# Optimization experiments

Hardware: AMD Instinct MI355X
Metric: run time of the kernel (lower is better)

## Reference

```python
import jax, jax.numpy as jnp
import numpy as np


def setup_inputs() -> dict:
    key = jax.random.key(0)
    ks = jax.random.split(key, 8)
    B, T, D, H, Z = 128, 512, 256, 1024, 128
    s_in = 1.0 / np.sqrt(D + H)
    s_h = 1.0 / np.sqrt(H)
    return {
        "x": jax.random.normal(ks[0], (B, T, D), jnp.float32),
        "W": jax.random.normal(ks[1], (D, 4 * H), jnp.float32) * s_in,
        "U": jax.random.normal(ks[2], (H, 4 * H), jnp.float32) * s_in,
        "b": jnp.zeros((4 * H,), jnp.float32),
        "Wm": jax.random.normal(ks[3], (H, Z), jnp.float32) * s_h,
        "bm": jnp.zeros((Z,), jnp.float32),
        "Wv": jax.random.normal(ks[4], (H, Z), jnp.float32) * s_h,
        "bv": jnp.zeros((Z,), jnp.float32),
        "eps": jax.random.normal(ks[5], (B, Z), jnp.float32),
    }


def reference(x, W, U, b, Wm, bm, Wv, bv, eps):
    # Keras LSTM with activation='softplus' (cell/output act), recurrent_activation=sigmoid.
    # Gate order in Keras kernels: i, f, c(g), o.
    B = x.shape[0]
    H = U.shape[0]

    def step(carry, xt):
        h, c = carry
        gates = xt @ W + h @ U + b  # [B, 4H]
        i, f, g, o = jnp.split(gates, 4, axis=-1)
        i = jax.nn.sigmoid(i)
        f = jax.nn.sigmoid(f)
        o = jax.nn.sigmoid(o)
        g = jax.nn.softplus(g)
        c_new = f * c + i * g
        h_new = o * jax.nn.softplus(c_new)
        return (h_new, c_new), None

    init = (jnp.zeros((B, H), x.dtype), jnp.zeros((B, H), x.dtype))
    (h_last, _), _ = jax.lax.scan(step, init, jnp.swapaxes(x, 0, 1))

    mu = h_last @ Wm + bm        # [B, Z]
    logvar = h_last @ Wv + bv    # [B, Z]
    z = mu + eps * jnp.exp(0.5 * logvar)  # reparameterization
    return mu, logvar, z
```

## Files before the change

kernel.cpp:

```cpp
#include <hip/hip_runtime.h>
#include <hip/hip_bf16.h>
#include <stdint.h>

#define NB 128
#define NT 512
#define ND 256
#define NH 1024
#define NZ 128
#define NG 4096

typedef __attribute__((ext_vector_type(8))) __bf16 bf16x8;
typedef __attribute__((ext_vector_type(4))) __bf16 bf16x4;
typedef __attribute__((ext_vector_type(4))) float floatx4;

__device__ __forceinline__ float fsigmoid_(float x) {
  return __fdividef(1.0f, 1.0f + __expf(-x));
}
__device__ __forceinline__ float fsoftplus_(float x) {
  return fmaxf(x, 0.0f) + __logf(1.0f + __expf(-fabsf(x)));
}

__device__ __forceinline__ bf16x8 load_bfrag(const float* s) {
  bf16x8 v;
#pragma unroll
  for (int jj = 0; jj < 8; ++jj) v[jj] = (__bf16)s[jj * NG];
  return v;
}

__global__ __launch_bounds__(256) void convert_x_kernel(
    const float4* __restrict__ x, __bf16* __restrict__ xb) {
  int i = blockIdx.x * 256 + threadIdx.x;
  int d4 = i & 63;
  int bt = i >> 6;
  int b = bt >> 9;
  int t = bt & 511;
  float4 v = x[i];
  bf16x4 o;
  o[0] = (__bf16)v.x; o[1] = (__bf16)v.y; o[2] = (__bf16)v.z; o[3] = (__bf16)v.w;
  *(bf16x4*)(xb + ((t * NB + b) * ND + d4 * 4)) = o;
}

__global__ __launch_bounds__(512, 1) void lstm_persistent(
    const __bf16* __restrict__ xb,
    const float* __restrict__ W,
    const float* __restrict__ U,
    const float* __restrict__ bias,
    __bf16* __restrict__ hbuf,
    float* __restrict__ hlast)
{
  const int tid = threadIdx.x;
  const int wg = blockIdx.x;
  const int m_blk = wg & 7;
  const int n_blk = wg >> 3;
  const int wave = tid >> 6;
  const int lane = tid & 63;
  const int q = lane >> 4;
  const int n16 = lane & 15;

  __shared__ float Gs[2][8][16][132];

#define AL(p) __hip_atomic_load(p, __ATOMIC_RELAXED, __HIP_MEMORY_SCOPE_AGENT)
#define AS(p, v) __hip_atomic_store(p, v, __ATOMIC_RELAXED, __HIP_MEMORY_SCOPE_AGENT)
#define MFMA_(a, b, acc) __builtin_amdgcn_mfma_f32_16x16x32_bf16(a, b, acc, 0, 0, 0)

  const int nb = n_blk * 32 + n16;
  const int c00 = nb,            c01 = nb + 16;
  const int c10 = NH + nb,       c11 = NH + nb + 16;
  const int c20 = 2 * NH + nb,   c21 = 2 * NH + nb + 16;
  const int c30 = 3 * NH + nb,   c31 = 3 * NH + nb + 16;

  const float* Wb = W + (wave * 32 + q * 8) * NG;
  bf16x8 BX00 = load_bfrag(Wb + c00), BX01 = load_bfrag(Wb + c01);
  bf16x8 BX10 = load_bfrag(Wb + c10), BX11 = load_bfrag(Wb + c11);
  bf16x8 BX20 = load_bfrag(Wb + c20), BX21 = load_bfrag(Wb + c21);
  bf16x8 BX30 = load_bfrag(Wb + c30), BX31 = load_bfrag(Wb + c31);
  const float* Ub = U + (wave * 128 + q * 8) * NG;
#define DECL_J(J)                                                       \
  bf16x8 BH00##J = load_bfrag(Ub + (J) * 32 * NG + c00);                \
  bf16x8 BH01##J = load_bfrag(Ub + (J) * 32 * NG + c01);                \
  bf16x8 BH10##J = load_bfrag(Ub + (J) * 32 * NG + c10);                \
  bf16x8 BH11##J = load_bfrag(Ub + (J) * 32 * NG + c11);                \
  bf16x8 BH20##J = load_bfrag(Ub + (J) * 32 * NG + c20);                \
  bf16x8 BH21##J = load_bfrag(Ub + (J) * 32 * NG + c21);                \
  bf16x8 BH30##J = load_bfrag(Ub + (J) * 32 * NG + c30);                \
  bf16x8 BH31##J = load_bfrag(Ub + (J) * 32 * NG + c31);
  DECL_J(0) DECL_J(1) DECL_J(2) DECL_J(3)
#undef DECL_J

  const float b00 = (wave == 0) ? bias[c00] : 0.f;
  const float b01 = (wave == 0) ? bias[c01] : 0.f;
  const float b10 = (wave == 0) ? bias[c10] : 0.f;
  const float b11 = (wave == 0) ? bias[c11] : 0.f;
  const float b20 = (wave == 0) ? bias[c20] : 0.f;
  const float b21 = (wave == 0) ? bias[c21] : 0.f;
  const float b30 = (wave == 0) ? bias[c30] : 0.f;
  const float b31 = (wave == 0) ? bias[c31] : 0.f;

  const int r_e = tid >> 5;
  const int c_e = tid & 31;
  const int hcol = n_blk * 32 + c_e;
  const int grow = m_blk * 16 + r_e;
  float c_state = 0.0f;

  const int goff = (m_blk * 16 + n16) * NH + (wave << 7) + (q << 3);

  floatx4 AC00, AC01, AC10, AC11, AC20, AC21, AC30, AC31;
#define XPHASE_(XA)                                                     \
  {                                                                     \
    AC00 = (floatx4){b00, b00, b00, b00}; AC01 = (floatx4){b01, b01, b01, b01}; \
    AC10 = (floatx4){b10, b10, b10, b10}; AC11 = (floatx4){b11, b11, b11, b11}; \
    AC20 = (floatx4){b20, b20, b20, b20}; AC21 = (floatx4){b21, b21, b21, b21}; \
    AC30 = (floatx4){b30, b30, b30, b30}; AC31 = (floatx4){b31, b31, b31, b31}; \
    AC00 = MFMA_(XA, BX00, AC00); AC01 = MFMA_(XA, BX01, AC01);         \
    AC10 = MFMA_(XA, BX10, AC10); AC11 = MFMA_(XA, BX11, AC11);         \
    AC20 = MFMA_(XA, BX20, AC20); AC21 = MFMA_(XA, BX21, AC21);         \
    AC30 = MFMA_(XA, BX30, AC30); AC31 = MFMA_(XA, BX31, AC31);         \
  }

#define XFRAG_PTR(T) (const bf16x8*)(xb + ((T) * NB + m_blk * 16 + n16) * ND \
                                     + wave * 32 + q * 8)

  {
    bf16x8 x0 = *XFRAG_PTR(0);
    XPHASE_(x0)
  }

  for (int t = 0; t < NT; ++t) {
    bf16x8 xv;
    if (t < NT - 1) xv = *XFRAG_PTR(t + 1);

    unsigned long long w0, w1, w2, w3, w4, w5, w6, w7;
    {
      const unsigned long long* hp =
          (const unsigned long long*)(hbuf + (t & 3) * (NB * NH) + goff);
      while (true) {
        w0 = AL(hp);      w1 = AL(hp + 1);
        w2 = AL(hp + 8);  w3 = AL(hp + 9);
        w4 = AL(hp + 16); w5 = AL(hp + 17);
        w6 = AL(hp + 24); w7 = AL(hp + 25);
        unsigned long long s =
            (w0 | w1 | w2 | w3 | w4 | w5 | w6 | w7) & 0x8000800080008000ULL;
        if (__all(s == 0ULL)) break;
        __builtin_amdgcn_s_sleep(1);
      }
    }
    union { unsigned long long u[2]; bf16x8 v; } u0, u1, u2, u3;
    u0.u[0] = w0; u0.u[1] = w1; u1.u[0] = w2; u1.u[1] = w3;
    u2.u[0] = w4; u2.u[1] = w5; u3.u[0] = w6; u3.u[1] = w7;
    bf16x8 a0 = u0.v, a1 = u1.v, a2 = u2.v, a3 = u3.v;

    AC00 = MFMA_(a0, BH000, AC00); AC01 = MFMA_(a0, BH010, AC01);
    AC10 = MFMA_(a0, BH100, AC10); AC11 = MFMA_(a0, BH110, AC11);
    AC20 = MFMA_(a0, BH200, AC20); AC21 = MFMA_(a0, BH210, AC21);
    AC30 = MFMA_(a0, BH300, AC30); AC31 = MFMA_(a0, BH310, AC31);
    AC00 = MFMA_(a1, BH001, AC00); AC01 = MFMA_(a1, BH011, AC01);
    AC10 = MFMA_(a1, BH101, AC10); AC11 = MFMA_(a1, BH111, AC11);
    AC20 = MFMA_(a1, BH201, AC20); AC21 = MFMA_(a1, BH211, AC21);
    AC30 = MFMA_(a1, BH301, AC30); AC31 = MFMA_(a1, BH311, AC31);
    AC00 = MFMA_(a2, BH002, AC00); AC01 = MFMA_(a2, BH012, AC01);
    AC10 = MFMA_(a2, BH102, AC10); AC11 = MFMA_(a2, BH112, AC11);
    AC20 = MFMA_(a2, BH202, AC20); AC21 = MFMA_(a2, BH212, AC21);
    AC30 = MFMA_(a2, BH302, AC30); AC31 = MFMA_(a2, BH312, AC31);
    AC00 = MFMA_(a3, BH003, AC00); AC01 = MFMA_(a3, BH013, AC01);
    AC10 = MFMA_(a3, BH103, AC10); AC11 = MFMA_(a3, BH113, AC11);
    AC20 = MFMA_(a3, BH203, AC20); AC21 = MFMA_(a3, BH213, AC21);
    AC30 = MFMA_(a3, BH303, AC30); AC31 = MFMA_(a3, BH313, AC31);

    const int gi = t & 1;
#pragma unroll
    for (int rr = 0; rr < 4; ++rr) {
      int row = q * 4 + rr;
      Gs[gi][wave][row][n16]       = AC00[rr];
      Gs[gi][wave][row][16 + n16]  = AC01[rr];
      Gs[gi][wave][row][32 + n16]  = AC10[rr];
      Gs[gi][wave][row][48 + n16]  = AC11[rr];
      Gs[gi][wave][row][64 + n16]  = AC20[rr];
      Gs[gi][wave][row][80 + n16]  = AC21[rr];
      Gs[gi][wave][row][96 + n16]  = AC30[rr];
      Gs[gi][wave][row][112 + n16] = AC31[rr];
    }

    __syncthreads();

    {
      float xi = 0.f, xf = 0.f, xg = 0.f, xo = 0.f;
#pragma unroll
      for (int w2i = 0; w2i < 8; ++w2i) {
        xi += Gs[gi][w2i][r_e][c_e];
        xf += Gs[gi][w2i][r_e][32 + c_e];
        xg += Gs[gi][w2i][r_e][64 + c_e];
        xo += Gs[gi][w2i][r_e][96 + c_e];
      }
      float iv = fsigmoid_(xi);
      float fv = fsigmoid_(xf);
      float gv = fsoftplus_(xg);
      float ov = fsigmoid_(xo);
      c_state = fv * c_state + iv * gv;
      float hv = ov * fsoftplus_(c_state);
      if (t == NT - 1) {
        hlast[grow * NH + hcol] = hv;
      } else {
        float hn1 = __shfl_xor(hv, 1);
        __hip_bfloat162 pk;
        pk.x = (__hip_bfloat16)hv; pk.y = (__hip_bfloat16)hn1;
        unsigned int pw = *(unsigned int*)&pk;
        unsigned int po = (unsigned int)__shfl_xor((int)pw, 2);
        if ((c_e & 3) == 0) {
          unsigned long long vv = ((unsigned long long)po << 32) | pw;
          AS((unsigned long long*)(hbuf + ((t + 1) & 3) * (NB * NH)
                                   + grow * NH + hcol), vv);
          AS((unsigned long long*)(hbuf + ((t + 3) & 3) * (NB * NH)
                                   + grow * NH + hcol),
             0xFFFFFFFFFFFFFFFFULL);
        }
      }
    }

    if (t < NT - 1) XPHASE_(xv)
  }
#undef XFRAG_PTR
#undef XPHASE_
#undef AS
#undef AL
#undef MFMA_
}

__global__ __launch_bounds__(128) void proj_kernel(
    const float* __restrict__ hlast,
    const float* __restrict__ Wm, const float* __restrict__ bm,
    const float* __restrict__ Wv, const float* __restrict__ bv,
    const float* __restrict__ eps, float* __restrict__ out) {
  __shared__ float hs[4][NH];
  const int bb = blockIdx.x * 4;
  for (int idx = threadIdx.x; idx < 4 * NH; idx += 128)
    hs[idx >> 10][idx & (NH - 1)] = hlast[(bb + (idx >> 10)) * NH + (idx & (NH - 1))];
  __syncthreads();
  const int z = threadIdx.x;
  float am[4] = {0.f, 0.f, 0.f, 0.f};
  float av[4] = {0.f, 0.f, 0.f, 0.f};
#pragma unroll 8
  for (int k = 0; k < NH; ++k) {
    float wm = Wm[k * NZ + z];
    float wv = Wv[k * NZ + z];
#pragma unroll
    for (int r = 0; r < 4; ++r) {
      am[r] += hs[r][k] * wm;
      av[r] += hs[r][k] * wv;
    }
  }
#pragma unroll
  for (int r = 0; r < 4; ++r) {
    int b = bb + r;
    float mu = am[r] + bm[z];
    float lv = av[r] + bv[z];
    float zz = mu + eps[b * NZ + z] * expf(0.5f * lv);
    out[b * NZ + z] = mu;
    out[NB * NZ + b * NZ + z] = lv;
    out[2 * NB * NZ + b * NZ + z] = zz;
  }
}

extern "C" void kernel_launch(void* const* d_in, const int* in_sizes, int n_in,
                              void* d_out, int out_size, void* d_ws, size_t ws_size,
                              hipStream_t stream) {
  const float* x   = (const float*)d_in[0];
  const float* W   = (const float*)d_in[1];
  const float* U   = (const float*)d_in[2];
  const float* b   = (const float*)d_in[3];
  const float* Wm  = (const float*)d_in[4];
  const float* bm  = (const float*)d_in[5];
  const float* Wv  = (const float*)d_in[6];
  const float* bv  = (const float*)d_in[7];
  const float* eps = (const float*)d_in[8];

  char* ws = (char*)d_ws;
  __bf16* hbuf = (__bf16*)ws;
  __bf16* xb   = (__bf16*)(ws + 1048576);
  float* hlast = (float*)(ws + 1048576);

  hipMemsetAsync(hbuf, 0, NB * NH * sizeof(__bf16), stream);
  hipMemsetAsync(hbuf + NB * NH, 0xFF, 3 * NB * NH * sizeof(__bf16), stream);

  convert_x_kernel<<<dim3((NB * NT * ND) / 4 / 256), dim3(256), 0, stream>>>(
      (const float4*)x, xb);

  void* args[] = {(void*)&xb, (void*)&W, (void*)&U, (void*)&b,
                  (void*)&hbuf, (void*)&hlast};
  hipLaunchCooperativeKernel(reinterpret_cast<void*>(lstm_persistent),
                             dim3(256), dim3(512), args, 0, stream);

  proj_kernel<<<dim3(32), dim3(128), 0, stream>>>(hlast, Wm, bm, Wv, bv, eps,
                                                  (float*)d_out);
}
```

Baseline: 2.415 ms.

## Split each workgroup's batch rows into two interleaved 8-row halves

Each workgroup now handles two 8-row batch groups (mA and mB) with separate accumulators and cell states, processing them one after the other within each timestep. While one half waits on its h dependency, the other half's producer group has time to finish, which is meant to hide cross-workgroup synchronization latency. Lanes with row index above 7 duplicate work in the MFMA (r8g = n16&7), so half the MFMA output is wasted. The polling loop also now reloads only the words still marked invalid. Costs include twice the accumulator registers and an extra __syncthreads per step.

```diff
diff --git a/kernel.cpp b/kernel.cpp
--- a/kernel.cpp
+++ b/kernel.cpp
@@ -50,14 +50,17 @@
 {
   const int tid = threadIdx.x;
   const int wg = blockIdx.x;
-  const int m_blk = wg & 7;
+  const int pp = wg & 7;
   const int n_blk = wg >> 3;
+  const int mA = pp;
+  const int mB = pp + 8;
   const int wave = tid >> 6;
   const int lane = tid & 63;
   const int q = lane >> 4;
   const int n16 = lane & 15;
-
-  __shared__ float Gs[2][8][16][132];
+  const int r8g = n16 & 7;
+
+  __shared__ float Gs[2][8][8][132];
 
 #define AL(p) __hip_atomic_load(p, __ATOMIC_RELAXED, __HIP_MEMORY_SCOPE_AGENT)
 #define AS(p, v) __hip_atomic_store(p, v, __ATOMIC_RELAXED, __HIP_MEMORY_SCOPE_AGENT)
@@ -96,130 +99,148 @@
   const float b30 = (wave == 0) ? bias[c30] : 0.f;
   const float b31 = (wave == 0) ? bias[c31] : 0.f;
 
-  const int r_e = tid >> 5;
-  const int c_e = tid & 31;
-  const int hcol = n_blk * 32 + c_e;
-  const int grow = m_blk * 16 + r_e;
-  float c_state = 0.0f;
-
-  const int goff = (m_blk * 16 + n16) * NH + (wave << 7) + (q << 3);
-
-  floatx4 AC00, AC01, AC10, AC11, AC20, AC21, AC30, AC31;
-#define XPHASE_(XA)                                                     \
+  float csA = 0.0f, csB = 0.0f;
+
+  floatx4 AA00, AA01, AA10, AA11, AA20, AA21, AA30, AA31;
+  floatx4 AB00, AB01, AB10, AB11, AB20, AB21, AB30, AB31;
+
+#define XPHASE_P(P, XA)                                                 \
   {                                                                     \
-    AC00 = (floatx4){b00, b00, b00, b00}; AC01 = (floatx4){b01, b01, b01, b01}; \
-    AC10 = (floatx4){b10, b10, b10, b10}; AC11 = (floatx4){b11, b11, b11, b11}; \
-    AC20 = (floatx4){b20, b20, b20, b20}; AC21 = (floatx4){b21, b21, b21, b21}; \
-    AC30 = (floatx4){b30, b30, b30, b30}; AC31 = (floatx4){b31, b31, b31, b31}; \
-    AC00 = MFMA_(XA, BX00, AC00); AC01 = MFMA_(XA, BX01, AC01);         \
-    AC10 = MFMA_(XA, BX10, AC10); AC11 = MFMA_(XA, BX11, AC11);         \
-    AC20 = MFMA_(XA, BX20, AC20); AC21 = MFMA_(XA, BX21, AC21);         \
-    AC30 = MFMA_(XA, BX30, AC30); AC31 = MFMA_(XA, BX31, AC31);         \
-  }
-
-#define XFRAG_PTR(T) (const bf16x8*)(xb + ((T) * NB + m_blk * 16 + n16) * ND \
-                                     + wave * 32 + q * 8)
+    P##00 = (floatx4){b00, b00, b00, b00}; P##01 = (floatx4){b01, b01, b01, b01}; \
+    P##10 = (floatx4){b10, b10, b10, b10}; P##11 = (floatx4){b11, b11, b11, b11}; \
+    P##20 = (floatx4){b20, b20, b20, b20}; P##21 = (floatx4){b21, b21, b21, b21}; \
+    P##30 = (floatx4){b30, b30, b30, b30}; P##31 = (floatx4){b31, b31, b31, b31}; \
+    P##00 = MFMA_(XA, BX00, P##00); P##01 = MFMA_(XA, BX01, P##01);     \
+    P##10 = MFMA_(XA, BX10, P##10); P##11 = MFMA_(XA, BX11, P##11);     \
+    P##20 = MFMA_(XA, BX20, P##20); P##21 = MFMA_(XA, BX21, P##21);     \
+    P##30 = MFMA_(XA, BX30, P##30); P##31 = MFMA_(XA, BX31, P##31);     \
+  }
+
+#define HMFMA_P(P, a0, a1, a2, a3)                                      \
+  {                                                                     \
+    P##00 = MFMA_(a0, BH000, P##00); P##01 = MFMA_(a0, BH010, P##01);   \
+    P##10 = MFMA_(a0, BH100, P##10); P##11 = MFMA_(a0, BH110, P##11);   \
+    P##20 = MFMA_(a0, BH200, P##20); P##21 = MFMA_(a0, BH210, P##21);   \
+    P##30 = MFMA_(a0, BH300, P##30); P##31 = MFMA_(a0, BH310, P##31);   \
+    P##00 = MFMA_(a1, BH001, P##00); P##01 = MFMA_(a1, BH011, P##01);   \
+    P##10 = MFMA_(a1, BH101, P##10); P##11 = MFMA_(a1, BH111, P##11);   \
+    P##20 = MFMA_(a1, BH201, P##20); P##21 = MFMA_(a1, BH211, P##21);   \
+    P##30 = MFMA_(a1, BH301, P##30); P##31 = MFMA_(a1, BH311, P##31);   \
+    P##00 = MFMA_(a2, BH002, P##00); P##01 = MFMA_(a2, BH012, P##01);   \
+    P##10 = MFMA_(a2, BH102, P##10); P##11 = MFMA_(a2, BH112, P##11);   \
+    P##20 = MFMA_(a2, BH202, P##20); P##21 = MFMA_(a2, BH212, P##21);   \
+    P##30 = MFMA_(a2, BH302, P##30); P##31 = MFMA_(a2, BH312, P##31);   \
+    P##00 = MFMA_(a3, BH003, P##00); P##01 = MFMA_(a3, BH013, P##01);   \
+    P##10 = MFMA_(a3, BH103, P##10); P##11 = MFMA_(a3, BH113, P##11);   \
+    P##20 = MFMA_(a3, BH203, P##20); P##21 = MFMA_(a3, BH213, P##21);   \
+    P##30 = MFMA_(a3, BH303, P##30); P##31 = MFMA_(a3, BH313, P##31);   \
+  }
+
+#define XFRAG_PTR(T, MG)                                                \
+  (const bf16x8*)(xb + ((T) * NB + (MG) * 8 + r8g) * ND + wave * 32 + q * 8)
+
+  const unsigned long long SGN = 0x8000800080008000ULL;
+
+#define HALF(G, MG, CS, P)                                              \
+  {                                                                     \
+    bf16x8 xv;                                                          \
+    if (t < NT - 1) xv = *XFRAG_PTR(t + 1, MG);                         \
+    unsigned long long w0 = SGN, w1 = SGN, w2 = SGN, w3 = SGN,          \
+                       w4 = SGN, w5 = SGN, w6 = SGN, w7 = SGN;          \
+    {                                                                   \
+      const unsigned long long* hp = (const unsigned long long*)        \
+          (hbuf + (t & 3) * (NB * NH) + ((MG) * 8 + r8g) * NH           \
+           + (wave << 7) + (q << 3));                                   \
+      while (true) {                                                    \
+        if (w0 & SGN) w0 = AL(hp);                                      \
+        if (w1 & SGN) w1 = AL(hp + 1);                                  \
+        if (w2 & SGN) w2 = AL(hp + 8);                                  \
+        if (w3 & SGN) w3 = AL(hp + 9);                                  \
+        if (w4 & SGN) w4 = AL(hp + 16);                                 \
+        if (w5 & SGN) w5 = AL(hp + 17);                                 \
+        if (w6 & SGN) w6 = AL(hp + 24);                                 \
+        if (w7 & SGN) w7 = AL(hp + 25);                                 \
+        unsigned long long s =                                          \
+            (w0 | w1 | w2 | w3 | w4 | w5 | w6 | w7) & SGN;              \
+        if (__all(s == 0ULL)) break;                                    \
+        __builtin_amdgcn_s_sleep(1);                                    \
+      }                                                                 \
+    }                                                                   \
+    union { unsigned long long u[2]; bf16x8 v; } u0, u1, u2, u3;        \
+    u0.u[0] = w0; u0.u[1] = w1; u1.u[0] = w2; u1.u[1] = w3;             \
+    u2.u[0] = w4; u2.u[1] = w5; u3.u[0] = w6; u3.u[1] = w7;             \
+    bf16x8 a0 = u0.v, a1 = u1.v, a2 = u2.v, a3 = u3.v;                  \
+    HMFMA_P(P, a0, a1, a2, a3)                                          \
+    if (q < 2) {                                                        \
+      _Pragma("unroll")                                                 \
+      for (int rr = 0; rr < 4; ++rr) {                                  \
+        int row = q * 4 + rr;                                           \
+        Gs[G][wave][row][n16]       = P##00[rr];                        \
+        Gs[G][wave][row][16 + n16]  = P##01[rr];                        \
+        Gs[G][wave][row][32 + n16]  = P##10[rr];                        \
+        Gs[G][wave][row][48 + n16]  = P##11[rr];                        \
+        Gs[G][wave][row][64 + n16]  = P##20[rr];                        \
+        Gs[G][wave][row][80 + n16]  = P##21[rr];                        \
+        Gs[G][wave][row][96 + n16]  = P##30[rr];                        \
+        Gs[G][wave][row][112 + n16] = P##31[rr];                        \
+      }                                                                 \
+    }                                                                   \
+    __syncthreads();                                                    \
+    if (tid < 256) {                                                    \
+      const int r8 = tid >> 5;                                          \
+      const int ce = tid & 31;                                          \
+      const int growx = (MG) * 8 + r8;                                  \
+      const int hc = n_blk * 32 + ce;                                   \
+      float xi = 0.f, xf = 0.f, xg = 0.f, xo = 0.f;                     \
+      _Pragma("unroll")                                                 \
+      for (int w2i = 0; w2i < 8; ++w2i) {                               \
+        xi += Gs[G][w2i][r8][ce];                                       \
+        xf += Gs[G][w2i][r8][32 + ce];                                  \
+        xg += Gs[G][w2i][r8][64 + ce];                                  \
+        xo += Gs[G][w2i][r8][96 + ce];                                  \
+      }                                                                 \
+      float iv = fsigmoid_(xi);                                         \
+      float fv = fsigmoid_(xf);                                         \
+      float gv = fsoftplus_(xg);                                        \
+      float ov = fsigmoid_(xo);                                         \
+      (CS) = fv * (CS) + iv * gv;                                       \
+      float hv = ov * fsoftplus_(CS);          \
+      if (t == NT - 1) {                                                \
+        hlast[growx * NH + hc] = hv;                                    \
+      } else {                                                          \
+        float hn1 = __shfl_xor(hv, 1);                                  \
+        __hip_bfloat162 pk;                                             \
+        pk.x = (__hip_bfloat16)hv; pk.y = (__hip_bfloat16)hn1;          \
+        unsigned int pw = *(unsigned int*)&pk;                          \
+        unsigned int po = (unsigned int)__shfl_xor((int)pw, 2);         \
+        if ((ce & 3) == 0) {                                            \
+          unsigned long long vv = ((unsigned long long)po << 32) | pw;  \
+          AS((unsigned long long*)(hbuf + ((t + 1) & 3) * (NB * NH)     \
+                                   + growx * NH + hc), vv);             \
+          AS((unsigned long long*)(hbuf + ((t + 3) & 3) * (NB * NH)     \
+                                   + growx * NH + hc),                  \
+             0xFFFFFFFFFFFFFFFFULL);                                    \
+        }                                                               \
+      }                                                                 \
+    }                                                                   \
+    if (t < NT - 1) XPHASE_P(P, xv)                                     \
+  }
 
   {
-    bf16x8 x0 = *XFRAG_PTR(0);
-    XPHASE_(x0)
+    bf16x8 x0a = *XFRAG_PTR(0, mA);
+    XPHASE_P(AA, x0a)
+    bf16x8 x0b = *XFRAG_PTR(0, mB);
+    XPHASE_P(AB, x0b)
   }
 
   for (int t = 0; t < NT; ++t) {
-    bf16x8 xv;
-    if (t < NT - 1) xv = *XFRAG_PTR(t + 1);
-
-    unsigned long long w0, w1, w2, w3, w4, w5, w6, w7;
-    {
-      const unsigned long long* hp =
-          (const unsigned long long*)(hbuf + (t & 3) * (NB * NH) + goff);
-      while (true) {
-        w0 = AL(hp);      w1 = AL(hp + 1);
-        w2 = AL(hp + 8);  w3 = AL(hp + 9);
-        w4 = AL(hp + 16); w5 = AL(hp + 17);
-        w6 = AL(hp + 24); w7 = AL(hp + 25);
-        unsigned long long s =
-            (w0 | w1 | w2 | w3 | w4 | w5 | w6 | w7) & 0x8000800080008000ULL;
-        if (__all(s == 0ULL)) break;
-        __builtin_amdgcn_s_sleep(1);
-      }
-    }
-    union { unsigned long long u[2]; bf16x8 v; } u0, u1, u2, u3;
-    u0.u[0] = w0; u0.u[1] = w1; u1.u[0] = w2; u1.u[1] = w3;
-    u2.u[0] = w4; u2.u[1] = w5; u3.u[0] = w6; u3.u[1] = w7;
-    bf16x8 a0 = u0.v, a1 = u1.v, a2 = u2.v, a3 = u3.v;
-
-    AC00 = MFMA_(a0, BH000, AC00); AC01 = MFMA_(a0, BH010, AC01);
-    AC10 = MFMA_(a0, BH100, AC10); AC11 = MFMA_(a0, BH110, AC11);
-    AC20 = MFMA_(a0, BH200, AC20); AC21 = MFMA_(a0, BH210, AC21);
-    AC30 = MFMA_(a0, BH300, AC30); AC31 = MFMA_(a0, BH310, AC31);
-    AC00 = MFMA_(a1, BH001, AC00); AC01 = MFMA_(a1, BH011, AC01);
-    AC10 = MFMA_(a1, BH101, AC10); AC11 = MFMA_(a1, BH111, AC11);
-    AC20 = MFMA_(a1, BH201, AC20); AC21 = MFMA_(a1, BH211, AC21);
-    AC30 = MFMA_(a1, BH301, AC30); AC31 = MFMA_(a1, BH311, AC31);
-    AC00 = MFMA_(a2, BH002, AC00); AC01 = MFMA_(a2, BH012, AC01);
-    AC10 = MFMA_(a2, BH102, AC10); AC11 = MFMA_(a2, BH112, AC11);
-    AC20 = MFMA_(a2, BH202, AC20); AC21 = MFMA_(a2, BH212, AC21);
-    AC30 = MFMA_(a2, BH302, AC30); AC31 = MFMA_(a2, BH312, AC31);
-    AC00 = MFMA_(a3, BH003, AC00); AC01 = MFMA_(a3, BH013, AC01);
-    AC10 = MFMA_(a3, BH103, AC10); AC11 = MFMA_(a3, BH113, AC11);
-    AC20 = MFMA_(a3, BH203, AC20); AC21 = MFMA_(a3, BH213, AC21);
-    AC30 = MFMA_(a3, BH303, AC30); AC31 = MFMA_(a3, BH313, AC31);
-
-    const int gi = t & 1;
-#pragma unroll
-    for (int rr = 0; rr < 4; ++rr) {
-      int row = q * 4 + rr;
-      Gs[gi][wave][row][n16]       = AC00[rr];
-      Gs[gi][wave][row][16 + n16]  = AC01[rr];
-      Gs[gi][wave][row][32 + n16]  = AC10[rr];
-      Gs[gi][wave][row][48 + n16]  = AC11[rr];
-      Gs[gi][wave][row][64 + n16]  = AC20[rr];
-      Gs[gi][wave][row][80 + n16]  = AC21[rr];
-      Gs[gi][wave][row][96 + n16]  = AC30[rr];
-      Gs[gi][wave][row][112 + n16] = AC31[rr];
-    }
-
-    __syncthreads();
-
-    {
-      float xi = 0.f, xf = 0.f, xg = 0.f, xo = 0.f;
-#pragma unroll
-      for (int w2i = 0; w2i < 8; ++w2i) {
-        xi += Gs[gi][w2i][r_e][c_e];
-        xf += Gs[gi][w2i][r_e][32 + c_e];
-        xg += Gs[gi][w2i][r_e][64 + c_e];
-        xo += Gs[gi][w2i][r_e][96 + c_e];
-      }
-      float iv = fsigmoid_(xi);
-      float fv = fsigmoid_(xf);
-      float gv = fsoftplus_(xg);
-      float ov = fsigmoid_(xo);
-      c_state = fv * c_state + iv * gv;
-      float hv = ov * fsoftplus_(c_state);
-      if (t == NT - 1) {
-        hlast[grow * NH + hcol] = hv;
-      } else {
-        float hn1 = __shfl_xor(hv, 1);
-        __hip_bfloat162 pk;
-        pk.x = (__hip_bfloat16)hv; pk.y = (__hip_bfloat16)hn1;
-        unsigned int pw = *(unsigned int*)&pk;
-        unsigned int po = (unsigned int)__shfl_xor((int)pw, 2);
-        if ((c_e & 3) == 0) {
-          unsigned long long vv = ((unsigned long long)po << 32) | pw;
-          AS((unsigned long long*)(hbuf + ((t + 1) & 3) * (NB * NH)
-                                   + grow * NH + hcol), vv);
-          AS((unsigned long long*)(hbuf + ((t + 3) & 3) * (NB * NH)
-                                   + grow * NH + hcol),
-             0xFFFFFFFFFFFFFFFFULL);
-        }
-      }
-    }
-
-    if (t < NT - 1) XPHASE_(xv)
-  }
+    HALF(0, mA, csA, AA)
+    HALF(1, mB, csB, AB)
+  }
+#undef HALF
 #undef XFRAG_PTR
-#undef XPHASE_
+#undef HMFMA_P
+#undef XPHASE_P
 #undef AS
 #undef AL
 #undef MFMA_
```

Result: slower. 7.259 ms (+200.6%).

## Prefetch next-step h poll loads and double-buffer spin polling per word

Applied to the files above, without the earlier changes.

Issues the atomic poll loads for the next timestep's h buffer before the input-projection MFMAs, so their latency overlaps that compute. The spin loop now alternates two in-flight load sets with no sleep and merges ready words one by one, keeping each 64-bit word once its sign bits show it is valid. This aims to cut the latency of the cross-workgroup recurrent barrier. The cost is more register pressure and more memory traffic while spinning. Merging per word also assumes each word is published atomically.

```diff
diff --git a/kernel.cpp b/kernel.cpp
--- a/kernel.cpp
+++ b/kernel.cpp
@@ -120,6 +120,26 @@
 #define XFRAG_PTR(T) (const bf16x8*)(xb + ((T) * NB + m_blk * 16 + n16) * ND \
                                      + wave * 32 + q * 8)
 
+  const unsigned long long SGN = 0x8000800080008000ULL;
+
+#define ISSUE_POLL(G)                                                   \
+    G##0 = AL(hp); G##1 = AL(hp + 1);                                   \
+    G##2 = AL(hp + 8); G##3 = AL(hp + 9);                                \
+    G##4 = AL(hp + 16); G##5 = AL(hp + 17);                              \
+    G##6 = AL(hp + 24); G##7 = AL(hp + 25);
+
+#define MERGE_POLL(G)                                                   \
+    if (m0 & SGN) m0 = G##0; if (m1 & SGN) m1 = G##1;                   \
+    if (m2 & SGN) m2 = G##2; if (m3 & SGN) m3 = G##3;                   \
+    if (m4 & SGN) m4 = G##4; if (m5 & SGN) m5 = G##5;                   \
+    if (m6 & SGN) m6 = G##6; if (m7 & SGN) m7 = G##7;
+
+#define POLL_DONE                                                       \
+    __all((((m0 | m1 | m2 | m3 | m4 | m5 | m6 | m7) & SGN) == 0ULL))
+
+  const unsigned long long* hp = (const unsigned long long*)(hbuf + goff);
+  unsigned long long A0, A1, A2, A3, A4, A5, A6, A7;
+  ISSUE_POLL(A)
   {
     bf16x8 x0 = *XFRAG_PTR(0);
     XPHASE_(x0)
@@ -129,24 +149,24 @@
     bf16x8 xv;
     if (t < NT - 1) xv = *XFRAG_PTR(t + 1);
 
-    unsigned long long w0, w1, w2, w3, w4, w5, w6, w7;
-    {
-      const unsigned long long* hp =
-          (const unsigned long long*)(hbuf + (t & 3) * (NB * NH) + goff);
+    unsigned long long m0 = SGN, m1 = SGN, m2 = SGN, m3 = SGN,
+                       m4 = SGN, m5 = SGN, m6 = SGN, m7 = SGN;
+    MERGE_POLL(A)
+    if (!POLL_DONE) {
+      unsigned long long B0, B1, B2, B3, B4, B5, B6, B7;
+      ISSUE_POLL(B)
       while (true) {
-        w0 = AL(hp);      w1 = AL(hp + 1);
-        w2 = AL(hp + 8);  w3 = AL(hp + 9);
-        w4 = AL(hp + 16); w5 = AL(hp + 17);
-        w6 = AL(hp + 24); w7 = AL(hp + 25);
-        unsigned long long s =
-            (w0 | w1 | w2 | w3 | w4 | w5 | w6 | w7) & 0x8000800080008000ULL;
-        if (__all(s == 0ULL)) break;
-        __builtin_amdgcn_s_sleep(1);
+        ISSUE_POLL(A)
+        MERGE_POLL(B)
+        if (POLL_DONE) break;
+        ISSUE_POLL(B)
+        MERGE_POLL(A)
+        if (POLL_DONE) break;
       }
     }
     union { unsigned long long u[2]; bf16x8 v; } u0, u1, u2, u3;
-    u0.u[0] = w0; u0.u[1] = w1; u1.u[0] = w2; u1.u[1] = w3;
-    u2.u[0] = w4; u2.u[1] = w5; u3.u[0] = w6; u3.u[1] = w7;
+    u0.u[0] = m0; u0.u[1] = m1; u1.u[0] = m2; u1.u[1] = m3;
+    u2.u[0] = m4; u2.u[1] = m5; u3.u[0] = m6; u3.u[1] = m7;
     bf16x8 a0 = u0.v, a1 = u1.v, a2 = u2.v, a3 = u3.v;
 
     AC00 = MFMA_(a0, BH000, AC00); AC01 = MFMA_(a0, BH010, AC01);
@@ -216,8 +236,15 @@
       }
     }
 
-    if (t < NT - 1) XPHASE_(xv)
-  }
+    if (t < NT - 1) {
+      hp = (const unsigned long long*)(hbuf + ((t + 1) & 3) * (NB * NH) + goff);
+      ISSUE_POLL(A)
+      XPHASE_(xv)
+    }
+  }
+#undef POLL_DONE
+#undef MERGE_POLL
+#undef ISSUE_POLL
 #undef XFRAG_PTR
 #undef XPHASE_
 #undef AS
```

Measured after the change: 3.344 ms. +38.5%, slower.

## Prefetch next-step hidden loads and consume h slices as they become ready

Applied to the files above, without the earlier changes.

The polling loads for the next timestep's hidden state are now issued before the input-projection MFMAs, so their latency overlaps that work. The wait loop also checks each of the four K-slices separately and runs its MFMAs as soon as that slice's sentinel bits clear. Only the words still marked not-ready are reloaded. This overlaps cross-block synchronization latency with compute, at the cost of more branching and wave-uniform votes in the spin loop, and possibly higher register pressure.

```diff
diff --git a/kernel.cpp b/kernel.cpp
--- a/kernel.cpp
+++ b/kernel.cpp
@@ -117,9 +117,31 @@
     AC30 = MFMA_(XA, BX30, AC30); AC31 = MFMA_(XA, BX31, AC31);         \
   }
 
+#define HSLICE(J, WA, WB)                                               \
+  {                                                                     \
+    union { unsigned long long u[2]; bf16x8 v; } uu;                    \
+    uu.u[0] = (WA); uu.u[1] = (WB);                                     \
+    bf16x8 aa = uu.v;                                                   \
+    AC00 = MFMA_(aa, BH00##J, AC00); AC01 = MFMA_(aa, BH01##J, AC01);   \
+    AC10 = MFMA_(aa, BH10##J, AC10); AC11 = MFMA_(aa, BH11##J, AC11);   \
+    AC20 = MFMA_(aa, BH20##J, AC20); AC21 = MFMA_(aa, BH21##J, AC21);   \
+    AC30 = MFMA_(aa, BH30##J, AC30); AC31 = MFMA_(aa, BH31##J, AC31);   \
+  }
+
 #define XFRAG_PTR(T) (const bf16x8*)(xb + ((T) * NB + m_blk * 16 + n16) * ND \
                                      + wave * 32 + q * 8)
 
+#define PRE_ISSUE()                                                     \
+    A0 = AL(hp); A1 = AL(hp + 1);                                       \
+    A2 = AL(hp + 8); A3 = AL(hp + 9);                                   \
+    A4 = AL(hp + 16); A5 = AL(hp + 17);                                 \
+    A6 = AL(hp + 24); A7 = AL(hp + 25);
+
+  const unsigned long long SGN = 0x8000800080008000ULL;
+
+  const unsigned long long* hp = (const unsigned long long*)(hbuf + goff);
+  unsigned long long A0, A1, A2, A3, A4, A5, A6, A7;
+  PRE_ISSUE()
   {
     bf16x8 x0 = *XFRAG_PTR(0);
     XPHASE_(x0)
@@ -129,42 +151,35 @@
     bf16x8 xv;
     if (t < NT - 1) xv = *XFRAG_PTR(t + 1);
 
-    unsigned long long w0, w1, w2, w3, w4, w5, w6, w7;
     {
-      const unsigned long long* hp =
-          (const unsigned long long*)(hbuf + (t & 3) * (NB * NH) + goff);
+      unsigned long long m0 = A0, m1 = A1, m2 = A2, m3 = A3,
+                         m4 = A4, m5 = A5, m6 = A6, m7 = A7;
+      bool d0 = false, d1 = false, d2 = false, d3 = false;
       while (true) {
-        w0 = AL(hp);      w1 = AL(hp + 1);
-        w2 = AL(hp + 8);  w3 = AL(hp + 9);
-        w4 = AL(hp + 16); w5 = AL(hp + 17);
-        w6 = AL(hp + 24); w7 = AL(hp + 25);
-        unsigned long long s =
-            (w0 | w1 | w2 | w3 | w4 | w5 | w6 | w7) & 0x8000800080008000ULL;
-        if (__all(s == 0ULL)) break;
+        if (!d0 && __all((int)(((m0 | m1) & SGN) == 0ULL))) {
+          d0 = true; HSLICE(0, m0, m1)
+        }
+        if (!d1 && __all((int)(((m2 | m3) & SGN) == 0ULL))) {
+          d1 = true; HSLICE(1, m2, m3)
+        }
+        if (!d2 && __all((int)(((m4 | m5) & SGN) == 0ULL))) {
+          d2 = true; HSLICE(2, m4, m5)
+        }
+        if (!d3 && __all((int)(((m6 | m7) & SGN) == 0ULL))) {
+          d3 = true; HSLICE(3, m6, m7)
+        }
+        if (d0 && d1 && d2 && d3) break;
         __builtin_amdgcn_s_sleep(1);
+        if (m0 & SGN) m0 = AL(hp);
+        if (m1 & SGN) m1 = AL(hp + 1);
+        if (m2 & SGN) m2 = AL(hp + 8);
+        if (m3 & SGN) m3 = AL(hp + 9);
+        if (m4 & SGN) m4 = AL(hp + 16);
+        if (m5 & SGN) m5 = AL(hp + 17);
+        if (m6 & SGN) m6 = AL(hp + 24);
+        if (m7 & SGN) m7 = AL(hp + 25);
       }
     }
-    union { unsigned long long u[2]; bf16x8 v; } u0, u1, u2, u3;
-    u0.u[0] = w0; u0.u[1] = w1; u1.u[0] = w2; u1.u[1] = w3;
-    u2.u[0] = w4; u2.u[1] = w5; u3.u[0] = w6; u3.u[1] = w7;
-    bf16x8 a0 = u0.v, a1 = u1.v, a2 = u2.v, a3 = u3.v;
-
-    AC00 = MFMA_(a0, BH000, AC00); AC01 = MFMA_(a0, BH010, AC01);
-    AC10 = MFMA_(a0, BH100, AC10); AC11 = MFMA_(a0, BH110, AC11);
-    AC20 = MFMA_(a0, BH200, AC20); AC21 = MFMA_(a0, BH210, AC21);
-    AC30 = MFMA_(a0, BH300, AC30); AC31 = MFMA_(a0, BH310, AC31);
-    AC00 = MFMA_(a1, BH001, AC00); AC01 = MFMA_(a1, BH011, AC01);
-    AC10 = MFMA_(a1, BH101, AC10); AC11 = MFMA_(a1, BH111, AC11);
-    AC20 = MFMA_(a1, BH201, AC20); AC21 = MFMA_(a1, BH211, AC21);
-    AC30 = MFMA_(a1, BH301, AC30); AC31 = MFMA_(a1, BH311, AC31);
-    AC00 = MFMA_(a2, BH002, AC00); AC01 = MFMA_(a2, BH012, AC01);
-    AC10 = MFMA_(a2, BH102, AC10); AC11 = MFMA_(a2, BH112, AC11);
-    AC20 = MFMA_(a2, BH202, AC20); AC21 = MFMA_(a2, BH212, AC21);
-    AC30 = MFMA_(a2, BH302, AC30); AC31 = MFMA_(a2, BH312, AC31);
-    AC00 = MFMA_(a3, BH003, AC00); AC01 = MFMA_(a3, BH013, AC01);
-    AC10 = MFMA_(a3, BH103, AC10); AC11 = MFMA_(a3, BH113, AC11);
-    AC20 = MFMA_(a3, BH203, AC20); AC21 = MFMA_(a3, BH213, AC21);
-    AC30 = MFMA_(a3, BH303, AC30); AC31 = MFMA_(a3, BH313, AC31);
 
     const int gi = t & 1;
 #pragma unroll
@@ -216,9 +231,15 @@
       }
     }
 
-    if (t < NT - 1) XPHASE_(xv)
-  }
+    if (t < NT - 1) {
+      hp = (const unsigned long long*)(hbuf + ((t + 1) & 3) * (NB * NH) + goff);
+      PRE_ISSUE()
+      XPHASE_(xv)
+    }
+  }
+#undef PRE_ISSUE
 #undef XFRAG_PTR
+#undef HSLICE
 #undef XPHASE_
 #undef AS
 #undef AL
```

After: 2.974 ms. 1.23x slower.
